# Performance work log

Hardware: AMD Instinct MI355X
Metric: run time of the kernel (lower is better)

The kernel has to match this reference:

```python
import jax, jax.numpy as jnp
import numpy as np

NUM_LEVELS = 16
FEAT = 4
BASE_RES = 16
MAX_RES = 2048
HSIZE = 1 << 22  # log2_hashmap_size = 22
HIDDEN = 64
PRIMES = np.array([1, 2654435761, 805459861], dtype=np.uint32)
GROWTH = np.exp((np.log(MAX_RES) - np.log(BASE_RES)) / (NUM_LEVELS - 1))


def _level_metas():
    # Mirrors torch-ngp gridencoder level setup (align_corners=False).
    metas, offset = [], 0
    for l in range(NUM_LEVELS):
        scale = BASE_RES * GROWTH ** l - 1.0
        res = int(np.ceil(scale)) + 1
        params = min(HSIZE, (res + 1) ** 3)
        params = int(np.ceil(params / 8) * 8)  # align to 8
        dense = (res + 1) ** 3 <= params       # dense index fits -> no hashing
        metas.append((float(scale), res, offset, params, dense))
        offset += params
    return metas, offset

METAS, TOTAL_PARAMS = _level_metas()
CORNERS = np.array([[(c >> d) & 1 for d in range(3)] for c in range(8)], dtype=np.uint32)  # [8,3]


def hashgrid_encode(pts, table):
    # pts: [N,3] in [0,1]; table: [TOTAL_PARAMS, FEAT]
    outs = []
    bits = CORNERS.astype(np.float32)  # [8,3]
    for scale, res, offset, params, dense in METAS:
        pos = pts * jnp.float32(scale) + 0.5          # align_corners=False offset
        pos_floor = jnp.floor(pos)
        frac = pos - pos_floor                        # [N,3]
        base = pos_floor.astype(jnp.uint32)           # [N,3]
        coords = base[:, None, :] + CORNERS[None]     # [N,8,3] uint32
        if dense:
            stride = np.uint32(res + 1)
            idx = coords[..., 0] + coords[..., 1] * stride + coords[..., 2] * stride * stride
        else:
            idx = (coords[..., 0] * PRIMES[0]) ^ (coords[..., 1] * PRIMES[1]) ^ (coords[..., 2] * PRIMES[2])
        idx = (idx % np.uint32(params)).astype(jnp.int32) + offset  # [N,8]
        # trilinear weights: prod_d (frac if corner bit else 1-frac)
        w = jnp.prod(jnp.where(bits[None], frac[:, None, :], 1.0 - frac[:, None, :]), axis=-1)  # [N,8]
        feats = table[idx]                            # [N,8,FEAT] gather
        outs.append(jnp.einsum('nc,ncf->nf', w, feats))
    return jnp.concatenate(outs, axis=-1)             # [N, NUM_LEVELS*FEAT]


def setup_inputs() -> dict:
    key = jax.random.key(0)
    k_x, k_t, k0, k1, k2 = jax.random.split(key, 5)
    N = 524288
    in_dim = NUM_LEVELS * FEAT  # 64
    x = jax.random.uniform(k_x, (N, 1, 3), dtype=jnp.float32)
    table = jax.random.uniform(k_t, (TOTAL_PARAMS, FEAT), dtype=jnp.float32, minval=-1e-4, maxval=1e-4)
    W0 = jax.random.normal(k0, (HIDDEN, in_dim), dtype=jnp.float32) / np.sqrt(in_dim)
    W1 = jax.random.normal(k1, (HIDDEN, HIDDEN), dtype=jnp.float32) / np.sqrt(HIDDEN)
    W2 = jax.random.normal(k2, (1, HIDDEN), dtype=jnp.float32) / np.sqrt(HIDDEN)
    return {"x": x, "table": table, "W0": W0, "W1": W1, "W2": W2}


def reference(x, table, W0, W1, W2):
    pts = x[:, 0]                       # n_encoders == 1
    h = hashgrid_encode(pts, table)     # [N, 64]
    h = jax.nn.relu(h @ W0.T)
    h = jax.nn.relu(h @ W1.T)
    return h @ W2.T                     # [N, 1] sdf (clip_sdf=None)
```

## Files before the change

### kernel.cpp

```cpp
#include <hip/hip_runtime.h>
#include <cmath>
#include <algorithm>

#define NLEVELS 16

typedef float v4f __attribute__((ext_vector_type(4)));

struct LevelMeta {
  float scale;
  unsigned stride;
  unsigned offset;
  unsigned mask;
  int hashed;
};
struct MetaPack { LevelMeta m[NLEVELS]; };

__global__ __launch_bounds__(256) void hg_encode_kernel(
    const float* __restrict__ x,
    const float* __restrict__ table,
    v4f* __restrict__ hb,
    MetaPack mp, int N, int pblocks)
{
  const int l = blockIdx.x / pblocks;
  const int p = (blockIdx.x - l * pblocks) * 256 + threadIdx.x;
  if (p >= N) return;

  const float    scale  = mp.m[l].scale;
  const unsigned stride = mp.m[l].stride;
  const unsigned offset = mp.m[l].offset;
  const unsigned mask   = mp.m[l].mask;
  const int      hashed = mp.m[l].hashed;

  const float px = x[3 * p + 0];
  const float py = x[3 * p + 1];
  const float pz = x[3 * p + 2];

  const float posx = px * scale + 0.5f;
  const float posy = py * scale + 0.5f;
  const float posz = pz * scale + 0.5f;
  const float flx = floorf(posx), fly = floorf(posy), flz = floorf(posz);
  const float fx = posx - flx, fy = posy - fly, fz = posz - flz;
  const unsigned bx = (unsigned)flx, by = (unsigned)fly, bz = (unsigned)flz;

  unsigned idx[8];
  if (hashed) {
    #pragma unroll
    for (int c = 0; c < 8; ++c) {
      const unsigned cx = bx + (c & 1);
      const unsigned cy = by + ((c >> 1) & 1);
      const unsigned cz = bz + ((c >> 2) & 1);
      idx[c] = ((cx ^ (cy * 2654435761u) ^ (cz * 805459861u)) & mask) + offset;
    }
  } else {
    #pragma unroll
    for (int c = 0; c < 8; ++c) {
      const unsigned cx = bx + (c & 1);
      const unsigned cy = by + ((c >> 1) & 1);
      const unsigned cz = bz + ((c >> 2) & 1);
      idx[c] = cx + cy * stride + cz * stride * stride + offset;
    }
  }

  v4f f[8];
  #pragma unroll
  for (int c = 0; c < 8; ++c)
    f[c] = ((const v4f*)table)[idx[c]];

  const float wx0 = 1.0f - fx, wx1 = fx;
  const float wy0 = 1.0f - fy, wy1 = fy;
  const float wz0 = 1.0f - fz, wz1 = fz;

  v4f acc = (v4f){0.f, 0.f, 0.f, 0.f};
  #pragma unroll
  for (int c = 0; c < 8; ++c) {
    const float w = ((c & 1) ? wx1 : wx0) *
                    ((c & 2) ? wy1 : wy0) *
                    ((c & 4) ? wz1 : wz0);
    acc += w * f[c];
  }

  __builtin_nontemporal_store(acc, &hb[(size_t)l * N + p]);
}

__global__ __launch_bounds__(128, 2) void mlp_kernel(
    const v4f* __restrict__ hb,
    const float* __restrict__ W0,
    const float* __restrict__ W1,
    const float* __restrict__ W2,
    float* __restrict__ out,
    int N)
{
  __shared__ float Hs[64 * 128];
  const int t = threadIdx.x;
  const int p = blockIdx.x * 128 + t;
  if (p >= N) return;

  float h[64];
  #pragma unroll
  for (int l = 0; l < NLEVELS; ++l) {
    const v4f v = __builtin_nontemporal_load(&hb[(size_t)l * N + p]);
    h[4 * l + 0] = v.x;
    h[4 * l + 1] = v.y;
    h[4 * l + 2] = v.z;
    h[4 * l + 3] = v.w;
  }

  #pragma unroll 2
  for (int j = 0; j < 64; ++j) {
    const float* __restrict__ wr = W0 + j * 64;
    float a0 = 0.f, a1 = 0.f, a2 = 0.f, a3 = 0.f;
    #pragma unroll
    for (int k = 0; k < 64; k += 4) {
      a0 += wr[k + 0] * h[k + 0];
      a1 += wr[k + 1] * h[k + 1];
      a2 += wr[k + 2] * h[k + 2];
      a3 += wr[k + 3] * h[k + 3];
    }
    Hs[j * 128 + t] = fmaxf((a0 + a1) + (a2 + a3), 0.f);
  }
  #pragma unroll
  for (int k = 0; k < 64; ++k) h[k] = Hs[k * 128 + t];

  #pragma unroll 2
  for (int j = 0; j < 64; ++j) {
    const float* __restrict__ wr = W1 + j * 64;
    float a0 = 0.f, a1 = 0.f, a2 = 0.f, a3 = 0.f;
    #pragma unroll
    for (int k = 0; k < 64; k += 4) {
      a0 += wr[k + 0] * h[k + 0];
      a1 += wr[k + 1] * h[k + 1];
      a2 += wr[k + 2] * h[k + 2];
      a3 += wr[k + 3] * h[k + 3];
    }
    Hs[j * 128 + t] = fmaxf((a0 + a1) + (a2 + a3), 0.f);
  }
  #pragma unroll
  for (int k = 0; k < 64; ++k) h[k] = Hs[k * 128 + t];

  {
    float a0 = 0.f, a1 = 0.f, a2 = 0.f, a3 = 0.f;
    #pragma unroll
    for (int k = 0; k < 64; k += 4) {
      a0 += W2[k + 0] * h[k + 0];
      a1 += W2[k + 1] * h[k + 1];
      a2 += W2[k + 2] * h[k + 2];
      a3 += W2[k + 3] * h[k + 3];
    }
    out[p] = (a0 + a1) + (a2 + a3);
  }
}

__global__ __launch_bounds__(128, 2) void sdf_fused_kernel(
    const float* __restrict__ x,
    const float* __restrict__ table,
    const float* __restrict__ W0,
    const float* __restrict__ W1,
    const float* __restrict__ W2,
    float* __restrict__ out,
    MetaPack mp, int N)
{
  __shared__ float Hs[64 * 128];
  const int t = threadIdx.x;
  const int p = blockIdx.x * 128 + t;
  if (p >= N) return;

  const float px = x[3 * p + 0];
  const float py = x[3 * p + 1];
  const float pz = x[3 * p + 2];

  float h[64];

  #pragma unroll
  for (int l = 0; l < NLEVELS; ++l) {
    const float    scale  = mp.m[l].scale;
    const unsigned stride = mp.m[l].stride;
    const unsigned offset = mp.m[l].offset;
    const unsigned mask   = mp.m[l].mask;
    const int      hashed = mp.m[l].hashed;

    const float posx = px * scale + 0.5f;
    const float posy = py * scale + 0.5f;
    const float posz = pz * scale + 0.5f;
    const float flx = floorf(posx), fly = floorf(posy), flz = floorf(posz);
    const float fx = posx - flx, fy = posy - fly, fz = posz - flz;
    const unsigned bx = (unsigned)flx, by = (unsigned)fly, bz = (unsigned)flz;

    unsigned idx[8];
    if (hashed) {
      #pragma unroll
      for (int c = 0; c < 8; ++c) {
        const unsigned cx = bx + (c & 1);
        const unsigned cy = by + ((c >> 1) & 1);
        const unsigned cz = bz + ((c >> 2) & 1);
        idx[c] = ((cx ^ (cy * 2654435761u) ^ (cz * 805459861u)) & mask) + offset;
      }
    } else {
      #pragma unroll
      for (int c = 0; c < 8; ++c) {
        const unsigned cx = bx + (c & 1);
        const unsigned cy = by + ((c >> 1) & 1);
        const unsigned cz = bz + ((c >> 2) & 1);
        idx[c] = cx + cy * stride + cz * stride * stride + offset;
      }
    }

    float4 f[8];
    #pragma unroll
    for (int c = 0; c < 8; ++c)
      f[c] = ((const float4*)table)[idx[c]];

    const float wx0 = 1.0f - fx, wx1 = fx;
    const float wy0 = 1.0f - fy, wy1 = fy;
    const float wz0 = 1.0f - fz, wz1 = fz;

    float a0 = 0.f, a1 = 0.f, a2 = 0.f, a3 = 0.f;
    #pragma unroll
    for (int c = 0; c < 8; ++c) {
      const float w = ((c & 1) ? wx1 : wx0) *
                      ((c & 2) ? wy1 : wy0) *
                      ((c & 4) ? wz1 : wz0);
      a0 += w * f[c].x;
      a1 += w * f[c].y;
      a2 += w * f[c].z;
      a3 += w * f[c].w;
    }
    h[4 * l + 0] = a0;
    h[4 * l + 1] = a1;
    h[4 * l + 2] = a2;
    h[4 * l + 3] = a3;
  }

  #pragma unroll 2
  for (int j = 0; j < 64; ++j) {
    const float* __restrict__ wr = W0 + j * 64;
    float a0 = 0.f, a1 = 0.f, a2 = 0.f, a3 = 0.f;
    #pragma unroll
    for (int k = 0; k < 64; k += 4) {
      a0 += wr[k + 0] * h[k + 0];
      a1 += wr[k + 1] * h[k + 1];
      a2 += wr[k + 2] * h[k + 2];
      a3 += wr[k + 3] * h[k + 3];
    }
    Hs[j * 128 + t] = fmaxf((a0 + a1) + (a2 + a3), 0.f);
  }
  #pragma unroll
  for (int k = 0; k < 64; ++k) h[k] = Hs[k * 128 + t];

  #pragma unroll 2
  for (int j = 0; j < 64; ++j) {
    const float* __restrict__ wr = W1 + j * 64;
    float a0 = 0.f, a1 = 0.f, a2 = 0.f, a3 = 0.f;
    #pragma unroll
    for (int k = 0; k < 64; k += 4) {
      a0 += wr[k + 0] * h[k + 0];
      a1 += wr[k + 1] * h[k + 1];
      a2 += wr[k + 2] * h[k + 2];
      a3 += wr[k + 3] * h[k + 3];
    }
    Hs[j * 128 + t] = fmaxf((a0 + a1) + (a2 + a3), 0.f);
  }
  #pragma unroll
  for (int k = 0; k < 64; ++k) h[k] = Hs[k * 128 + t];

  {
    float a0 = 0.f, a1 = 0.f, a2 = 0.f, a3 = 0.f;
    #pragma unroll
    for (int k = 0; k < 64; k += 4) {
      a0 += W2[k + 0] * h[k + 0];
      a1 += W2[k + 1] * h[k + 1];
      a2 += W2[k + 2] * h[k + 2];
      a3 += W2[k + 3] * h[k + 3];
    }
    out[p] = (a0 + a1) + (a2 + a3);
  }
}

extern "C" void kernel_launch(void* const* d_in, const int* in_sizes, int n_in,
                              void* d_out, int out_size, void* d_ws, size_t ws_size,
                              hipStream_t stream)
{
  const float* x  = (const float*)d_in[0];
  const float* tb = (const float*)d_in[1];
  const float* W0 = (const float*)d_in[2];
  const float* W1 = (const float*)d_in[3];
  const float* W2 = (const float*)d_in[4];
  float* out = (float*)d_out;
  const int N = out_size;

  MetaPack mp;
  const double growth = std::exp((std::log(2048.0) - std::log(16.0)) / 15.0);
  unsigned long long offset = 0;
  for (int l = 0; l < NLEVELS; ++l) {
    const double scale = 16.0 * std::pow(growth, (double)l) - 1.0;
    const int res = (int)std::ceil(scale) + 1;
    const long long cube = (long long)(res + 1) * (res + 1) * (res + 1);
    long long params = std::min((long long)(1 << 22), cube);
    params = ((params + 7) / 8) * 8;
    const bool dense = (cube <= params);
    mp.m[l].scale  = (float)scale;
    mp.m[l].stride = (unsigned)(res + 1);
    mp.m[l].offset = (unsigned)offset;
    mp.m[l].mask   = (unsigned)(params - 1);
    mp.m[l].hashed = dense ? 0 : 1;
    offset += (unsigned long long)params;
  }

  const size_t need = (size_t)N * 64 * sizeof(float);
  if (d_ws != nullptr && ws_size >= need) {
    const int pblocks = (N + 255) / 256;
    hipLaunchKernelGGL(hg_encode_kernel, dim3(NLEVELS * pblocks), dim3(256), 0,
                       stream, x, tb, (v4f*)d_ws, mp, N, pblocks);
    hipLaunchKernelGGL(mlp_kernel, dim3((N + 127) / 128), dim3(128), 0, stream,
                       (const v4f*)d_ws, W0, W1, W2, out, N);
  } else {
    const int grid = (N + 127) / 128;
    hipLaunchKernelGGL(sdf_fused_kernel, dim3(grid), dim3(128), 0, stream,
                       x, tb, W0, W1, W2, out, mp, N);
  }
}
```

Measured before the change: 1.533 ms.

## Restructure MLP kernel so each lane owns a neuron with weights in registers

The MLP kernel now maps each wave's 64 lanes to the 64 output neurons and processes 8 points per wave. Each lane keeps one weight row in registers, and the point activations are staged in LDS and read as broadcasts. The final layer becomes a cross-lane shuffle reduction. The aim is to replace per-thread scalar weight streaming and per-thread 64-wide hidden state with register-resident weights. In exchange, every wave reloads the full weight matrices for only 8 points and adds LDS traffic and barriers.

```diff
diff --git a/kernel.cpp b/kernel.cpp
--- a/kernel.cpp
+++ b/kernel.cpp
@@ -82,7 +82,7 @@
   __builtin_nontemporal_store(acc, &hb[(size_t)l * N + p]);
 }
 
-__global__ __launch_bounds__(128, 2) void mlp_kernel(
+__global__ __launch_bounds__(256, 2) void mlp_kernel(
     const v4f* __restrict__ hb,
     const float* __restrict__ W0,
     const float* __restrict__ W1,
@@ -90,64 +90,98 @@
     float* __restrict__ out,
     int N)
 {
-  __shared__ float Hs[64 * 128];
-  const int t = threadIdx.x;
-  const int p = blockIdx.x * 128 + t;
-  if (p >= N) return;
-
-  float h[64];
-  #pragma unroll
-  for (int l = 0; l < NLEVELS; ++l) {
-    const v4f v = __builtin_nontemporal_load(&hb[(size_t)l * N + p]);
-    h[4 * l + 0] = v.x;
-    h[4 * l + 1] = v.y;
-    h[4 * l + 2] = v.z;
-    h[4 * l + 3] = v.w;
-  }
-
-  #pragma unroll 2
-  for (int j = 0; j < 64; ++j) {
-    const float* __restrict__ wr = W0 + j * 64;
-    float a0 = 0.f, a1 = 0.f, a2 = 0.f, a3 = 0.f;
-    #pragma unroll
-    for (int k = 0; k < 64; k += 4) {
-      a0 += wr[k + 0] * h[k + 0];
-      a1 += wr[k + 1] * h[k + 1];
-      a2 += wr[k + 2] * h[k + 2];
-      a3 += wr[k + 3] * h[k + 3];
-    }
-    Hs[j * 128 + t] = fmaxf((a0 + a1) + (a2 + a3), 0.f);
-  }
-  #pragma unroll
-  for (int k = 0; k < 64; ++k) h[k] = Hs[k * 128 + t];
-
-  #pragma unroll 2
-  for (int j = 0; j < 64; ++j) {
-    const float* __restrict__ wr = W1 + j * 64;
-    float a0 = 0.f, a1 = 0.f, a2 = 0.f, a3 = 0.f;
-    #pragma unroll
-    for (int k = 0; k < 64; k += 4) {
-      a0 += wr[k + 0] * h[k + 0];
-      a1 += wr[k + 1] * h[k + 1];
-      a2 += wr[k + 2] * h[k + 2];
-      a3 += wr[k + 3] * h[k + 3];
-    }
-    Hs[j * 128 + t] = fmaxf((a0 + a1) + (a2 + a3), 0.f);
-  }
-  #pragma unroll
-  for (int k = 0; k < 64; ++k) h[k] = Hs[k * 128 + t];
-
+  __shared__ float ls[4 * 2 * 8 * 68];
+  const int tid  = threadIdx.x;
+  const int lane = tid & 63;
+  const int wave = tid >> 6;
+  float* __restrict__ h0 = &ls[wave * (2 * 8 * 68)];
+  float* __restrict__ h1 = h0 + 8 * 68;
+
+  const int pbase = blockIdx.x * 32 + wave * 8;
+
+  #pragma unroll
+  for (int t = 0; t < 2; ++t) {
+    const int flat = t * 64 + lane;
+    const int l = flat >> 3;
+    const int p = flat & 7;
+    const int gp = pbase + p;
+    v4f v = (v4f){0.f, 0.f, 0.f, 0.f};
+    if (gp < N) v = hb[(size_t)l * N + gp];
+    *(v4f*)&h0[p * 68 + l * 4] = v;
+  }
+
+  float w[64];
   {
-    float a0 = 0.f, a1 = 0.f, a2 = 0.f, a3 = 0.f;
-    #pragma unroll
-    for (int k = 0; k < 64; k += 4) {
-      a0 += W2[k + 0] * h[k + 0];
-      a1 += W2[k + 1] * h[k + 1];
-      a2 += W2[k + 2] * h[k + 2];
-      a3 += W2[k + 3] * h[k + 3];
-    }
-    out[p] = (a0 + a1) + (a2 + a3);
-  }
+    const v4f* __restrict__ wr = (const v4f*)(W0 + lane * 64);
+    #pragma unroll
+    for (int q = 0; q < 16; ++q) {
+      const v4f wv = wr[q];
+      w[4 * q + 0] = wv.x; w[4 * q + 1] = wv.y;
+      w[4 * q + 2] = wv.z; w[4 * q + 3] = wv.w;
+    }
+  }
+
+  __syncthreads();
+
+  float acc[8];
+  #pragma unroll
+  for (int p = 0; p < 8; ++p) {
+    float a = 0.f;
+    #pragma unroll
+    for (int q = 0; q < 16; ++q) {
+      const v4f hv = *(const v4f*)&h0[p * 68 + q * 4];
+      a += hv.x * w[4 * q + 0];
+      a += hv.y * w[4 * q + 1];
+      a += hv.z * w[4 * q + 2];
+      a += hv.w * w[4 * q + 3];
+    }
+    acc[p] = fmaxf(a, 0.f);
+  }
+
+  #pragma unroll
+  for (int p = 0; p < 8; ++p) h1[p * 68 + lane] = acc[p];
+
+  {
+    const v4f* __restrict__ wr = (const v4f*)(W1 + lane * 64);
+    #pragma unroll
+    for (int q = 0; q < 16; ++q) {
+      const v4f wv = wr[q];
+      w[4 * q + 0] = wv.x; w[4 * q + 1] = wv.y;
+      w[4 * q + 2] = wv.z; w[4 * q + 3] = wv.w;
+    }
+  }
+
+  __syncthreads();
+
+  float acc2[8];
+  #pragma unroll
+  for (int p = 0; p < 8; ++p) {
+    float a = 0.f;
+    #pragma unroll
+    for (int q = 0; q < 16; ++q) {
+      const v4f hv = *(const v4f*)&h1[p * 68 + q * 4];
+      a += hv.x * w[4 * q + 0];
+      a += hv.y * w[4 * q + 1];
+      a += hv.z * w[4 * q + 2];
+      a += hv.w * w[4 * q + 3];
+    }
+    acc2[p] = fmaxf(a, 0.f);
+  }
+
+  const float w2 = W2[lane];
+  float myout = 0.f;
+  #pragma unroll
+  for (int p = 0; p < 8; ++p) {
+    float v = acc2[p] * w2;
+    v += __shfl_xor(v, 1);
+    v += __shfl_xor(v, 2);
+    v += __shfl_xor(v, 4);
+    v += __shfl_xor(v, 8);
+    v += __shfl_xor(v, 16);
+    v += __shfl_xor(v, 32);
+    if (lane == p) myout = v;
+  }
+  if (lane < 8 && (pbase + lane) < N) out[pbase + lane] = myout;
 }
 
 __global__ __launch_bounds__(128, 2) void sdf_fused_kernel(
@@ -310,7 +344,8 @@
     const int pblocks = (N + 255) / 256;
     hipLaunchKernelGGL(hg_encode_kernel, dim3(NLEVELS * pblocks), dim3(256), 0,
                        stream, x, tb, (v4f*)d_ws, mp, N, pblocks);
-    hipLaunchKernelGGL(mlp_kernel, dim3((N + 127) / 128), dim3(128), 0, stream,
+    const int mblocks = (N + 31) / 32;
+    hipLaunchKernelGGL(mlp_kernel, dim3(mblocks), dim3(256), 0, stream,
                        (const v4f*)d_ws, W0, W1, W2, out, N);
   } else {
     const int grid = (N + 127) / 128;
```

Result: faster. 1.375 ms (-10.3%).
